# Kernel optimization log

Hardware: AMD Instinct MI355X
Metric: run time of the kernel (lower is better)

The kernel has to match this reference:

```python
import jax, jax.numpy as jnp
import numpy as np

ENC_DIM, DEC_DIM, ATT_DIM = 2048, 512, 512

def setup_inputs() -> dict:
    key = jax.random.key(0)
    ks = jax.random.split(key, 8)
    s_enc = 1.0 / np.sqrt(ENC_DIM)
    s_dec = 1.0 / np.sqrt(DEC_DIM)
    s_att = 1.0 / np.sqrt(ATT_DIM)
    return {
        "encoder_out": jax.random.normal(ks[0], (256, 196, ENC_DIM), jnp.float32),
        "decoder_hidden": jax.random.normal(ks[1], (256, DEC_DIM), jnp.float32),
        "W_enc": jax.random.uniform(ks[2], (ENC_DIM, ATT_DIM), jnp.float32, -s_enc, s_enc),
        "b_enc": jax.random.uniform(ks[3], (ATT_DIM,), jnp.float32, -s_enc, s_enc),
        "W_dec": jax.random.uniform(ks[4], (DEC_DIM, ATT_DIM), jnp.float32, -s_dec, s_dec),
        "b_dec": jax.random.uniform(ks[5], (ATT_DIM,), jnp.float32, -s_dec, s_dec),
        "W_att": jax.random.uniform(ks[6], (ATT_DIM, 1), jnp.float32, -s_att, s_att),
        "b_att": jax.random.uniform(ks[7], (1,), jnp.float32, -s_att, s_att),
    }

def reference(encoder_out, decoder_hidden, W_enc, b_enc, W_dec, b_dec, W_att, b_att):
    # att1: (B, P, A); att2: (B, 1, A)
    att1 = jnp.einsum('bpe,ea->bpa', encoder_out, W_enc) + b_enc
    att2 = (decoder_hidden @ W_dec + b_dec)[:, None, :]
    # scalar score per pixel: (B, P)
    e = (jax.nn.relu(att1 + att2) @ W_att)[..., 0] + b_att[0]
    alpha = jax.nn.softmax(e, axis=-1)  # softmax over pixels
    z = jnp.einsum('bpe,bp->be', encoder_out, alpha)
    return (z, alpha)
```

## Files before the change

### kernel.cpp

```cpp
#include <hip/hip_runtime.h>
#include <hip/hip_bf16.h>

#define ENC_DIM 2048
#define DEC_DIM 512
#define ATT_DIM 512
#define NB 256
#define NP 196
#define M_TOT (NB * NP)
#define BM 64
#define BK 32
#define NSTEP (ENC_DIM / BK)

typedef __attribute__((ext_vector_type(8))) short short8;
typedef __attribute__((ext_vector_type(4))) short short4s;
typedef __attribute__((ext_vector_type(4))) float f32x4;

__device__ __forceinline__ short4s cvt4(f32x4 v) {
    union { short4s s; __hip_bfloat16 h[4]; } u;
    u.h[0] = __float2bfloat16(v[0]);
    u.h[1] = __float2bfloat16(v[1]);
    u.h[2] = __float2bfloat16(v[2]);
    u.h[3] = __float2bfloat16(v[3]);
    return u.s;
}

__global__ __launch_bounds__(256) void prep_kernel(const float* __restrict__ W,
                                                   __hip_bfloat16* __restrict__ Btt,
                                                   const float* __restrict__ dec,
                                                   const float* __restrict__ W_dec,
                                                   const float* __restrict__ b_dec,
                                                   const float* __restrict__ b_enc,
                                                   float* __restrict__ att2f) {
    __shared__ float ds[DEC_DIM];
    if (blockIdx.x < 512) {
        const int gid = blockIdx.x * 256 + threadIdx.x;
        const int s   = gid >> 11;
        const int u   = gid & 2047;
        const int fr  = u >> 6;
        const int kg  = (u >> 4) & 3;
        const int l15 = u & 15;
        const int col = fr * 16 + l15;
        const int k0  = s * 32 + kg * 8;
        union { short8 v; __hip_bfloat16 h[8]; } x;
        #pragma unroll
        for (int i = 0; i < 8; ++i)
            x.h[i] = __float2bfloat16(W[(size_t)(k0 + i) * ATT_DIM + col]);
        *(short8*)((short*)Btt + (size_t)gid * 8) = x.v;
    } else {
        const int b = blockIdx.x - 512;
        const int t = threadIdx.x;
        ds[t]       = dec[(size_t)b * DEC_DIM + t];
        ds[t + 256] = dec[(size_t)b * DEC_DIM + t + 256];
        __syncthreads();
        #pragma unroll
        for (int j = 0; j < 2; ++j) {
            const int n = t + j * 256;
            float s = 0.f;
            #pragma unroll 8
            for (int k = 0; k < DEC_DIM; ++k)
                s += ds[k] * W_dec[(size_t)k * ATT_DIM + n];
            att2f[(size_t)b * ATT_DIM + n] = s + b_dec[n] + b_enc[n];
        }
    }
}

__global__ __launch_bounds__(512, 4) void e_kernel(const float* __restrict__ enc,
                                                   const short* __restrict__ Btt,
                                                   const float* __restrict__ att2f,
                                                   const float* __restrict__ W_att,
                                                   float* __restrict__ e_out) {
    __shared__ __attribute__((aligned(16))) short As[2][2048];
    __shared__ float ebuf[8][64];

    const int tid  = threadIdx.x;
    const int lane = tid & 63;
    const int wv   = tid >> 6;
    const int l15  = lane & 15;
    const int kg   = lane >> 4;
    const int M0   = blockIdx.x * BM;

    const int arow = tid >> 3;
    const int aq   = tid & 7;
    const float* asrc = enc + (size_t)(M0 + arow) * ENC_DIM + aq * 4;
    const int awr = (arow >> 4) * 512 + (aq >> 1) * 128 + (arow & 15) * 8 + (aq & 1) * 4;

    const short* pBb = Btt + wv * 2048 + kg * 128 + l15 * 8;

    f32x4 acc[4][4];
    #pragma unroll
    for (int i = 0; i < 4; ++i)
        #pragma unroll
        for (int j = 0; j < 4; ++j)
            acc[i][j] = (f32x4){0.f, 0.f, 0.f, 0.f};

    *(short4s*)&As[0][awr] = cvt4(*(const f32x4*)asrc);
    f32x4 avP = *(const f32x4*)(asrc + BK);
    asm volatile("s_waitcnt lgkmcnt(0)" ::: "memory");
    __builtin_amdgcn_s_barrier();

    const short* Ac = &As[0][0];
    short*       An = &As[1][0];

    for (int s = 0; s < NSTEP; ++s) {
        const short* pbs = pBb + (size_t)s * 16384;
        const short8 c0 = *(const short8*)(pbs);
        const short8 c1 = *(const short8*)(pbs + 512);
        const short8 c2 = *(const short8*)(pbs + 1024);
        const short8 c3 = *(const short8*)(pbs + 1536);
        f32x4 avN = *(const f32x4*)(asrc + (size_t)((s + 2) & 63) * BK);
        __builtin_amdgcn_sched_barrier(0);

        __builtin_amdgcn_s_setprio(1);
        {
            const short8 a0 = *(const short8*)&Ac[0 * 512 + lane * 8];
            acc[0][0] = __builtin_amdgcn_mfma_f32_16x16x32_bf16(a0, c0, acc[0][0], 0, 0, 0);
            acc[0][1] = __builtin_amdgcn_mfma_f32_16x16x32_bf16(a0, c1, acc[0][1], 0, 0, 0);
            acc[0][2] = __builtin_amdgcn_mfma_f32_16x16x32_bf16(a0, c2, acc[0][2], 0, 0, 0);
            acc[0][3] = __builtin_amdgcn_mfma_f32_16x16x32_bf16(a0, c3, acc[0][3], 0, 0, 0);
        }
        {
            const short8 a1 = *(const short8*)&Ac[1 * 512 + lane * 8];
            acc[1][0] = __builtin_amdgcn_mfma_f32_16x16x32_bf16(a1, c0, acc[1][0], 0, 0, 0);
            acc[1][1] = __builtin_amdgcn_mfma_f32_16x16x32_bf16(a1, c1, acc[1][1], 0, 0, 0);
            acc[1][2] = __builtin_amdgcn_mfma_f32_16x16x32_bf16(a1, c2, acc[1][2], 0, 0, 0);
            acc[1][3] = __builtin_amdgcn_mfma_f32_16x16x32_bf16(a1, c3, acc[1][3], 0, 0, 0);
        }
        {
            const short8 a2 = *(const short8*)&Ac[2 * 512 + lane * 8];
            acc[2][0] = __builtin_amdgcn_mfma_f32_16x16x32_bf16(a2, c0, acc[2][0], 0, 0, 0);
            acc[2][1] = __builtin_amdgcn_mfma_f32_16x16x32_bf16(a2, c1, acc[2][1], 0, 0, 0);
            acc[2][2] = __builtin_amdgcn_mfma_f32_16x16x32_bf16(a2, c2, acc[2][2], 0, 0, 0);
            acc[2][3] = __builtin_amdgcn_mfma_f32_16x16x32_bf16(a2, c3, acc[2][3], 0, 0, 0);
        }
        {
            const short8 a3 = *(const short8*)&Ac[3 * 512 + lane * 8];
            acc[3][0] = __builtin_amdgcn_mfma_f32_16x16x32_bf16(a3, c0, acc[3][0], 0, 0, 0);
            acc[3][1] = __builtin_amdgcn_mfma_f32_16x16x32_bf16(a3, c1, acc[3][1], 0, 0, 0);
            acc[3][2] = __builtin_amdgcn_mfma_f32_16x16x32_bf16(a3, c2, acc[3][2], 0, 0, 0);
            acc[3][3] = __builtin_amdgcn_mfma_f32_16x16x32_bf16(a3, c3, acc[3][3], 0, 0, 0);
        }
        __builtin_amdgcn_s_setprio(0);

        *(short4s*)&An[awr] = cvt4(avP);
        avP = avN;
        asm volatile("s_waitcnt lgkmcnt(0)" ::: "memory");
        __builtin_amdgcn_s_barrier();
        const short* tmp = Ac; Ac = An; An = (short*)tmp;
    }

    float wat[4];
    #pragma unroll
    for (int nf = 0; nf < 4; ++nf) wat[nf] = W_att[wv * 64 + nf * 16 + l15];

    #pragma unroll
    for (int mf = 0; mf < 4; ++mf) {
        #pragma unroll
        for (int rr = 0; rr < 4; ++rr) {
            const int ml = mf * 16 + kg * 4 + rr;
            const int bb = (M0 + ml) / NP;
            const float* arow2 = att2f + (size_t)bb * ATT_DIM + wv * 64 + l15;
            float sv = 0.f;
            #pragma unroll
            for (int nf = 0; nf < 4; ++nf) {
                float v = acc[mf][nf][rr] + arow2[nf * 16];
                sv += fmaxf(v, 0.f) * wat[nf];
            }
            sv += __shfl_xor(sv, 1);
            sv += __shfl_xor(sv, 2);
            sv += __shfl_xor(sv, 4);
            sv += __shfl_xor(sv, 8);
            if (l15 == 0) ebuf[wv][ml] = sv;
        }
    }
    __syncthreads();
    if (tid < 64) {
        float sv = 0.f;
        #pragma unroll
        for (int w = 0; w < 8; ++w) sv += ebuf[w][tid];
        e_out[M0 + tid] = sv;
    }
}

__global__ __launch_bounds__(256) void z_kernel(const float* __restrict__ enc,
                                                const float* __restrict__ e,
                                                float* __restrict__ z,
                                                float* __restrict__ alpha) {
    const int b  = blockIdx.x;
    const int cb = blockIdx.y;
    const int t  = threadIdx.x;
    __shared__ float al[NP];
    __shared__ float red[4];

    float ev = (t < NP) ? e[(size_t)b * NP + t] : -1e30f;
    float m = ev;
    #pragma unroll
    for (int o = 32; o > 0; o >>= 1) m = fmaxf(m, __shfl_xor(m, o));
    if ((t & 63) == 0) red[t >> 6] = m;
    __syncthreads();
    m = fmaxf(fmaxf(red[0], red[1]), fmaxf(red[2], red[3]));
    __syncthreads();
    float ex = (t < NP) ? __expf(ev - m) : 0.f;
    float s = ex;
    #pragma unroll
    for (int o = 32; o > 0; o >>= 1) s += __shfl_xor(s, o);
    if ((t & 63) == 0) red[t >> 6] = s;
    __syncthreads();
    s = red[0] + red[1] + red[2] + red[3];
    const float a = ex * (1.0f / s);
    if (t < NP) {
        al[t] = a;
        if (cb == 0) alpha[(size_t)b * NP + t] = a;
    }
    __syncthreads();

    const int c0 = cb * 1024 + t * 4;
    const float4* ep = (const float4*)(enc + (size_t)b * NP * ENC_DIM + c0);
    float4 z0 = make_float4(0.f, 0.f, 0.f, 0.f);
    float4 z1 = make_float4(0.f, 0.f, 0.f, 0.f);
    #pragma unroll 4
    for (int p = 0; p < NP; p += 2) {
        const float a0 = al[p];
        const float a1 = al[p + 1];
        const float4 v0 = ep[(size_t)p * (ENC_DIM / 4)];
        const float4 v1 = ep[(size_t)(p + 1) * (ENC_DIM / 4)];
        z0.x += a0 * v0.x; z0.y += a0 * v0.y; z0.z += a0 * v0.z; z0.w += a0 * v0.w;
        z1.x += a1 * v1.x; z1.y += a1 * v1.y; z1.z += a1 * v1.z; z1.w += a1 * v1.w;
    }
    z0.x += z1.x; z0.y += z1.y; z0.z += z1.z; z0.w += z1.w;
    *(float4*)(z + (size_t)b * ENC_DIM + c0) = z0;
}

extern "C" void kernel_launch(void* const* d_in, const int* in_sizes, int n_in,
                              void* d_out, int out_size, void* d_ws, size_t ws_size,
                              hipStream_t stream) {
    const float* enc   = (const float*)d_in[0];
    const float* dec   = (const float*)d_in[1];
    const float* W_enc = (const float*)d_in[2];
    const float* b_enc = (const float*)d_in[3];
    const float* W_dec = (const float*)d_in[4];
    const float* b_dec = (const float*)d_in[5];
    const float* W_att = (const float*)d_in[6];

    float* z     = (float*)d_out;
    float* alpha = z + (size_t)NB * ENC_DIM;

    char* ws = (char*)d_ws;
    __hip_bfloat16* Btt = (__hip_bfloat16*)ws;
    float* att2f        = (float*)(ws + 2 * 1024 * 1024);
    float* e            = (float*)(ws + 2 * 1024 * 1024 + 512 * 1024);

    prep_kernel<<<768, 256, 0, stream>>>(W_enc, Btt, dec, W_dec, b_dec, b_enc, att2f);
    e_kernel<<<M_TOT / BM, 512, 0, stream>>>(enc, (const short*)Btt, att2f, W_att, e);
    z_kernel<<<dim3(NB, 2), 256, 0, stream>>>(enc, e, z, alpha);
}
```

Before: 298.9 us.

## Fuse score GEMM, softmax and weighted sum into one per-batch kernel

Replaces the separate e_kernel and z_kernel with a single kernel that runs one block per batch element. The block computes scores for all 196 pixels in two M-chunks (112 and 84 rows), then does the softmax and the weighted sum over encoder_out in the same block, so the intermediate score buffer and one launch go away. The grid shrinks from 784 blocks to 256, which may leave the GPU underfilled, and the chunks pad up to 208 rows. The z pass now uses 512 threads per batch instead of two 256-thread blocks.

```diff
diff --git a/kernel.cpp b/kernel.cpp
--- a/kernel.cpp
+++ b/kernel.cpp
@@ -6,22 +6,23 @@
 #define ATT_DIM 512
 #define NB 256
 #define NP 196
-#define M_TOT (NB * NP)
-#define BM 64
 #define BK 32
 #define NSTEP (ENC_DIM / BK)
 
 typedef __attribute__((ext_vector_type(8))) short short8;
-typedef __attribute__((ext_vector_type(4))) short short4s;
 typedef __attribute__((ext_vector_type(4))) float f32x4;
 
-__device__ __forceinline__ short4s cvt4(f32x4 v) {
-    union { short4s s; __hip_bfloat16 h[4]; } u;
-    u.h[0] = __float2bfloat16(v[0]);
-    u.h[1] = __float2bfloat16(v[1]);
-    u.h[2] = __float2bfloat16(v[2]);
-    u.h[3] = __float2bfloat16(v[3]);
-    return u.s;
+__device__ __forceinline__ short8 cvt8v(f32x4 x, f32x4 y) {
+    union { short8 v; __hip_bfloat16 h[8]; } u;
+    u.h[0] = __float2bfloat16(x[0]);
+    u.h[1] = __float2bfloat16(x[1]);
+    u.h[2] = __float2bfloat16(x[2]);
+    u.h[3] = __float2bfloat16(x[3]);
+    u.h[4] = __float2bfloat16(y[0]);
+    u.h[5] = __float2bfloat16(y[1]);
+    u.h[6] = __float2bfloat16(y[2]);
+    u.h[7] = __float2bfloat16(y[3]);
+    return u.v;
 }
 
 __global__ __launch_bounds__(256) void prep_kernel(const float* __restrict__ W,
@@ -64,37 +65,42 @@
     }
 }
 
-__global__ __launch_bounds__(512, 4) void e_kernel(const float* __restrict__ enc,
-                                                   const short* __restrict__ Btt,
-                                                   const float* __restrict__ att2f,
-                                                   const float* __restrict__ W_att,
-                                                   float* __restrict__ e_out) {
-    __shared__ __attribute__((aligned(16))) short As[2][2048];
-    __shared__ float ebuf[8][64];
-
-    const int tid  = threadIdx.x;
+template<int MF>
+__device__ __forceinline__ void run_chunk(const float* __restrict__ encB,
+                                          const short* __restrict__ Btt,
+                                          const float* __restrict__ att2b,
+                                          const float* __restrict__ W_att,
+                                          short (*As)[4096],
+                                          float (*ebuf)[128],
+                                          float* e_lds,
+                                          int prow0, int tid) {
     const int lane = tid & 63;
     const int wv   = tid >> 6;
     const int l15  = lane & 15;
     const int kg   = lane >> 4;
-    const int M0   = blockIdx.x * BM;
-
-    const int arow = tid >> 3;
-    const int aq   = tid & 7;
-    const float* asrc = enc + (size_t)(M0 + arow) * ENC_DIM + aq * 4;
-    const int awr = (arow >> 4) * 512 + (aq >> 1) * 128 + (arow & 15) * 8 + (aq & 1) * 4;
+
+    const int srow = tid >> 2;
+    const int p    = prow0 + srow;
+    const int cp   = p > (NP - 1) ? (NP - 1) : p;
+    const float* asrc = encB + (size_t)cp * ENC_DIM + (tid & 3) * 8;
+    const int awr = (srow >> 4) * 512 + (tid & 3) * 128 + (srow & 15) * 8;
 
     const short* pBb = Btt + wv * 2048 + kg * 128 + l15 * 8;
 
-    f32x4 acc[4][4];
-    #pragma unroll
-    for (int i = 0; i < 4; ++i)
+    f32x4 acc[MF][4];
+    #pragma unroll
+    for (int i = 0; i < MF; ++i)
         #pragma unroll
         for (int j = 0; j < 4; ++j)
             acc[i][j] = (f32x4){0.f, 0.f, 0.f, 0.f};
 
-    *(short4s*)&As[0][awr] = cvt4(*(const f32x4*)asrc);
-    f32x4 avP = *(const f32x4*)(asrc + BK);
+    {
+        f32x4 lo = *(const f32x4*)asrc;
+        f32x4 hi = *(const f32x4*)(asrc + 4);
+        *(short8*)&As[0][awr] = cvt8v(lo, hi);
+    }
+    f32x4 avPa = *(const f32x4*)(asrc + BK);
+    f32x4 avPb = *(const f32x4*)(asrc + BK + 4);
     asm volatile("s_waitcnt lgkmcnt(0)" ::: "memory");
     __builtin_amdgcn_s_barrier();
 
@@ -107,42 +113,23 @@
         const short8 c1 = *(const short8*)(pbs + 512);
         const short8 c2 = *(const short8*)(pbs + 1024);
         const short8 c3 = *(const short8*)(pbs + 1536);
-        f32x4 avN = *(const f32x4*)(asrc + (size_t)((s + 2) & 63) * BK);
+        f32x4 avNa = *(const f32x4*)(asrc + (size_t)((s + 2) & 63) * BK);
+        f32x4 avNb = *(const f32x4*)(asrc + (size_t)((s + 2) & 63) * BK + 4);
         __builtin_amdgcn_sched_barrier(0);
 
         __builtin_amdgcn_s_setprio(1);
-        {
-            const short8 a0 = *(const short8*)&Ac[0 * 512 + lane * 8];
-            acc[0][0] = __builtin_amdgcn_mfma_f32_16x16x32_bf16(a0, c0, acc[0][0], 0, 0, 0);
-            acc[0][1] = __builtin_amdgcn_mfma_f32_16x16x32_bf16(a0, c1, acc[0][1], 0, 0, 0);
-            acc[0][2] = __builtin_amdgcn_mfma_f32_16x16x32_bf16(a0, c2, acc[0][2], 0, 0, 0);
-            acc[0][3] = __builtin_amdgcn_mfma_f32_16x16x32_bf16(a0, c3, acc[0][3], 0, 0, 0);
-        }
-        {
-            const short8 a1 = *(const short8*)&Ac[1 * 512 + lane * 8];
-            acc[1][0] = __builtin_amdgcn_mfma_f32_16x16x32_bf16(a1, c0, acc[1][0], 0, 0, 0);
-            acc[1][1] = __builtin_amdgcn_mfma_f32_16x16x32_bf16(a1, c1, acc[1][1], 0, 0, 0);
-            acc[1][2] = __builtin_amdgcn_mfma_f32_16x16x32_bf16(a1, c2, acc[1][2], 0, 0, 0);
-            acc[1][3] = __builtin_amdgcn_mfma_f32_16x16x32_bf16(a1, c3, acc[1][3], 0, 0, 0);
-        }
-        {
-            const short8 a2 = *(const short8*)&Ac[2 * 512 + lane * 8];
-            acc[2][0] = __builtin_amdgcn_mfma_f32_16x16x32_bf16(a2, c0, acc[2][0], 0, 0, 0);
-            acc[2][1] = __builtin_amdgcn_mfma_f32_16x16x32_bf16(a2, c1, acc[2][1], 0, 0, 0);
-            acc[2][2] = __builtin_amdgcn_mfma_f32_16x16x32_bf16(a2, c2, acc[2][2], 0, 0, 0);
-            acc[2][3] = __builtin_amdgcn_mfma_f32_16x16x32_bf16(a2, c3, acc[2][3], 0, 0, 0);
-        }
-        {
-            const short8 a3 = *(const short8*)&Ac[3 * 512 + lane * 8];
-            acc[3][0] = __builtin_amdgcn_mfma_f32_16x16x32_bf16(a3, c0, acc[3][0], 0, 0, 0);
-            acc[3][1] = __builtin_amdgcn_mfma_f32_16x16x32_bf16(a3, c1, acc[3][1], 0, 0, 0);
-            acc[3][2] = __builtin_amdgcn_mfma_f32_16x16x32_bf16(a3, c2, acc[3][2], 0, 0, 0);
-            acc[3][3] = __builtin_amdgcn_mfma_f32_16x16x32_bf16(a3, c3, acc[3][3], 0, 0, 0);
+        #pragma unroll
+        for (int mf = 0; mf < MF; ++mf) {
+            const short8 a = *(const short8*)&Ac[mf * 512 + lane * 8];
+            acc[mf][0] = __builtin_amdgcn_mfma_f32_16x16x32_bf16(a, c0, acc[mf][0], 0, 0, 0);
+            acc[mf][1] = __builtin_amdgcn_mfma_f32_16x16x32_bf16(a, c1, acc[mf][1], 0, 0, 0);
+            acc[mf][2] = __builtin_amdgcn_mfma_f32_16x16x32_bf16(a, c2, acc[mf][2], 0, 0, 0);
+            acc[mf][3] = __builtin_amdgcn_mfma_f32_16x16x32_bf16(a, c3, acc[mf][3], 0, 0, 0);
         }
         __builtin_amdgcn_s_setprio(0);
 
-        *(short4s*)&An[awr] = cvt4(avP);
-        avP = avN;
+        *(short8*)&An[awr] = cvt8v(avPa, avPb);
+        avPa = avNa; avPb = avNb;
         asm volatile("s_waitcnt lgkmcnt(0)" ::: "memory");
         __builtin_amdgcn_s_barrier();
         const short* tmp = Ac; Ac = An; An = (short*)tmp;
@@ -151,14 +138,13 @@
     float wat[4];
     #pragma unroll
     for (int nf = 0; nf < 4; ++nf) wat[nf] = W_att[wv * 64 + nf * 16 + l15];
-
-    #pragma unroll
-    for (int mf = 0; mf < 4; ++mf) {
+    const float* arow2 = att2b + wv * 64 + l15;
+
+    #pragma unroll
+    for (int mf = 0; mf < MF; ++mf) {
         #pragma unroll
         for (int rr = 0; rr < 4; ++rr) {
             const int ml = mf * 16 + kg * 4 + rr;
-            const int bb = (M0 + ml) / NP;
-            const float* arow2 = att2f + (size_t)bb * ATT_DIM + wv * 64 + l15;
             float sv = 0.f;
             #pragma unroll
             for (int nf = 0; nf < 4; ++nf) {
@@ -173,51 +159,67 @@
         }
     }
     __syncthreads();
-    if (tid < 64) {
+    if (tid < MF * 16) {
         float sv = 0.f;
         #pragma unroll
         for (int w = 0; w < 8; ++w) sv += ebuf[w][tid];
-        e_out[M0 + tid] = sv;
-    }
-}
-
-__global__ __launch_bounds__(256) void z_kernel(const float* __restrict__ enc,
-                                                const float* __restrict__ e,
-                                                float* __restrict__ z,
-                                                float* __restrict__ alpha) {
-    const int b  = blockIdx.x;
-    const int cb = blockIdx.y;
-    const int t  = threadIdx.x;
+        const int pp = prow0 + tid;
+        if (pp < NP) e_lds[pp] = sv;
+    }
+    __syncthreads();
+}
+
+__global__ __launch_bounds__(512, 2) void fused_kernel(const float* __restrict__ enc,
+                                                       const short* __restrict__ Btt,
+                                                       const float* __restrict__ att2f,
+                                                       const float* __restrict__ W_att,
+                                                       float* __restrict__ z,
+                                                       float* __restrict__ alpha) {
+    __shared__ __attribute__((aligned(16))) short As[2][4096];
+    __shared__ float ebuf[8][128];
+    __shared__ float e_lds[NP];
     __shared__ float al[NP];
-    __shared__ float red[4];
-
-    float ev = (t < NP) ? e[(size_t)b * NP + t] : -1e30f;
+    __shared__ float red[8];
+
+    const int tid = threadIdx.x;
+    const int b   = blockIdx.x;
+    const float* encB  = enc + (size_t)b * NP * ENC_DIM;
+    const float* att2b = att2f + (size_t)b * ATT_DIM;
+
+    run_chunk<7>(encB, Btt, att2b, W_att, As, ebuf, e_lds, 0,   tid);
+    run_chunk<6>(encB, Btt, att2b, W_att, As, ebuf, e_lds, 112, tid);
+
+    const int lane = tid & 63;
+    const int wv   = tid >> 6;
+    float ev = (tid < NP) ? e_lds[tid] : -1e30f;
     float m = ev;
     #pragma unroll
     for (int o = 32; o > 0; o >>= 1) m = fmaxf(m, __shfl_xor(m, o));
-    if ((t & 63) == 0) red[t >> 6] = m;
-    __syncthreads();
-    m = fmaxf(fmaxf(red[0], red[1]), fmaxf(red[2], red[3]));
-    __syncthreads();
-    float ex = (t < NP) ? __expf(ev - m) : 0.f;
-    float s = ex;
-    #pragma unroll
-    for (int o = 32; o > 0; o >>= 1) s += __shfl_xor(s, o);
-    if ((t & 63) == 0) red[t >> 6] = s;
-    __syncthreads();
-    s = red[0] + red[1] + red[2] + red[3];
-    const float a = ex * (1.0f / s);
-    if (t < NP) {
-        al[t] = a;
-        if (cb == 0) alpha[(size_t)b * NP + t] = a;
-    }
-    __syncthreads();
-
-    const int c0 = cb * 1024 + t * 4;
-    const float4* ep = (const float4*)(enc + (size_t)b * NP * ENC_DIM + c0);
+    if (lane == 0) red[wv] = m;
+    __syncthreads();
+    m = red[0];
+    #pragma unroll
+    for (int w = 1; w < 8; ++w) m = fmaxf(m, red[w]);
+    __syncthreads();
+    float ex = (tid < NP) ? __expf(ev - m) : 0.f;
+    float sum = ex;
+    #pragma unroll
+    for (int o = 32; o > 0; o >>= 1) sum += __shfl_xor(sum, o);
+    if (lane == 0) red[wv] = sum;
+    __syncthreads();
+    sum = red[0] + red[1] + red[2] + red[3] + red[4] + red[5] + red[6] + red[7];
+    const float a = ex * (1.0f / sum);
+    if (tid < NP) {
+        al[tid] = a;
+        alpha[(size_t)b * NP + tid] = a;
+    }
+    __syncthreads();
+
+    const int c0 = tid * 4;
+    const float4* ep = (const float4*)(encB + c0);
     float4 z0 = make_float4(0.f, 0.f, 0.f, 0.f);
     float4 z1 = make_float4(0.f, 0.f, 0.f, 0.f);
-    #pragma unroll 4
+    #pragma unroll 2
     for (int p = 0; p < NP; p += 2) {
         const float a0 = al[p];
         const float a1 = al[p + 1];
@@ -247,9 +249,7 @@
     char* ws = (char*)d_ws;
     __hip_bfloat16* Btt = (__hip_bfloat16*)ws;
     float* att2f        = (float*)(ws + 2 * 1024 * 1024);
-    float* e            = (float*)(ws + 2 * 1024 * 1024 + 512 * 1024);
 
     prep_kernel<<<768, 256, 0, stream>>>(W_enc, Btt, dec, W_dec, b_dec, b_enc, att2f);
-    e_kernel<<<M_TOT / BM, 512, 0, stream>>>(enc, (const short*)Btt, att2f, W_att, e);
-    z_kernel<<<dim3(NB, 2), 256, 0, stream>>>(enc, e, z, alpha);
-}
+    fused_kernel<<<NB, 512, 0, stream>>>(enc, (const short*)Btt, att2f, W_att, z, alpha);
+}
```

After: 288.3 us. 1.04x faster.
